# Optimization experiments

Measured on AMD Instinct MI355X. Metric: run time of the kernel, lower is better.

The kernel has to match this reference:

```python
import jax, jax.numpy as jnp
import numpy as np

BETA = 0.25

def setup_inputs() -> dict:
    key = jax.random.key(0)
    k1, k2 = jax.random.split(key)
    z = jax.random.normal(k1, (32, 256, 32, 32), dtype=jnp.float32)
    # embedding init ~ U(-1/K, 1/K) as intended by the module
    K, D = 1024, 256
    codebook = jax.random.uniform(k2, (K, D), dtype=jnp.float32, minval=-1.0 / K, maxval=1.0 / K)
    return {"z": z, "codebook": codebook}


def reference(z, codebook):
    # z: [B, D, H, W] -> [B, H, W, D]
    zt = jnp.transpose(z, (0, 2, 3, 1))
    B, H, W, D = zt.shape
    z_flat = zt.reshape(-1, D)  # [N, D]
    # pairwise squared distance: ||z||^2 + ||e||^2 - 2 z e^T
    dist = (
        jnp.sum(z_flat * z_flat, axis=1, keepdims=True)
        + jnp.sum(codebook * codebook, axis=1)[None, :]
        - 2.0 * jnp.matmul(z_flat, codebook.T)
    )  # [N, K]
    idx = jnp.argmin(dist, axis=1)  # [N]
    z_q = codebook[idx].reshape(B, H, W, D)
    sg = jax.lax.stop_gradient
    loss = jnp.mean((sg(z_q) - zt) ** 2) + BETA * jnp.mean((sg(zt) - z_q) ** 2)
    # straight-through estimator
    z_q = zt + sg(z_q - zt)
    z_q = jnp.transpose(z_q, (0, 3, 1, 2))  # back to [B, D, H, W]
    return z_q, idx, loss
```

## Files before the change

### kernel.cpp

```cpp
#include <hip/hip_runtime.h>


#define D_DIM   256
#define K_CODES 1024
#define HW      1024
#define MT      128
#define NT      256
#define BK      16
#define THREADS 512

#define ZQ_OFF   0
#define IDX_OFF  8388608
#define LOSS_OFF 8421376

#define SMEM_FLOATS (D_DIM*MT + BK*NT + MT + MT)
#define SMEM_BYTES  (SMEM_FLOATS * 4)

extern __shared__ float smem[];

__global__ void enorm_kernel(const float* __restrict__ cb, float* __restrict__ enorm) {
    int gt = blockIdx.x * blockDim.x + threadIdx.x;
    int k = gt >> 6;
    int lane = gt & 63;
    const float4* row = (const float4*)(cb + (size_t)k * D_DIM);
    float4 v = row[lane];
    float s = fmaf(v.x, v.x, fmaf(v.y, v.y, fmaf(v.z, v.z, v.w * v.w)));
    #pragma unroll
    for (int off = 32; off; off >>= 1) s += __shfl_xor(s, off);
    if (lane == 0) enorm[k] = s;
}

__global__ __launch_bounds__(THREADS, 2) void vq_kernel(
        const float* __restrict__ z, const float* __restrict__ cb,
        const float* __restrict__ enorm, float* __restrict__ out)
{
    float* As = smem;
    float* Es = smem + D_DIM * MT;
    int*   bestm   = (int*)(smem + D_DIM*MT + BK*NT);
    float* znorm_s = (float*)(smem + D_DIM*MT + BK*NT + MT);

    const int t   = threadIdx.x;
    const int blk = blockIdx.x;
    const int b   = blk >> 3;
    const int p0  = (blk & 7) * MT;
    const float* zb = z + (size_t)b * D_DIM * HW;

    for (int i = t; i < D_DIM * MT / 4; i += THREADS) {
        int d = i >> 5, m4 = i & 31;
        *(float4*)(As + d * MT + m4 * 4) = *(const float4*)(zb + d * HW + p0 + m4 * 4);
    }
    __syncthreads();

    {
        int m = t & (MT - 1), q = t >> 7;
        const float* col = As + m;
        double zp = 0.0;
        #pragma unroll 8
        for (int d = q * 64; d < q * 64 + 64; ++d) {
            double v = (double)col[d * MT];
            zp += v * v;
        }
        double* zscr = (double*)Es;
        zscr[q * MT + m] = zp;
    }
    __syncthreads();
    if (t < MT) {
        double* zscr = (double*)Es;
        double s = (zscr[t] + zscr[MT + t]) + (zscr[2 * MT + t] + zscr[3 * MT + t]);
        znorm_s[t] = (float)s;
    }
    __syncthreads();

    const int tx = t & 31, ty = t >> 5;
    const int m_base = ty * 8;
    const int kx = tx * 8;

    float znf[8];
    #pragma unroll
    for (int i = 0; i < 8; ++i) znf[i] = znorm_s[m_base + i];

    float bestv[8]; int besti[8];
    #pragma unroll
    for (int i = 0; i < 8; ++i) { bestv[i] = 3.4e38f; besti[i] = 0; }

    for (int c = 0; c < 4; ++c) {
        const int k0 = c * NT;
        float acc[8][8];
        #pragma unroll
        for (int i = 0; i < 8; ++i)
            #pragma unroll
            for (int j = 0; j < 8; ++j) acc[i][j] = 0.f;

        for (int dk = 0; dk < D_DIM; dk += BK) {
            __syncthreads();
            for (int i = t; i < BK * NT / 4; i += THREADS) {
                int kk = i >> 2, d4 = i & 3;
                float4 v = *(const float4*)(cb + (size_t)(k0 + kk) * D_DIM + dk + d4 * 4);
                Es[(d4 * 4 + 0) * NT + kk] = v.x;
                Es[(d4 * 4 + 1) * NT + kk] = v.y;
                Es[(d4 * 4 + 2) * NT + kk] = v.z;
                Es[(d4 * 4 + 3) * NT + kk] = v.w;
            }
            __syncthreads();
            #pragma unroll
            for (int dd = 0; dd < BK; ++dd) {
                float a[8], e[8];
                *(float4*)(a)     = *(const float4*)(As + (dk + dd) * MT + m_base);
                *(float4*)(a + 4) = *(const float4*)(As + (dk + dd) * MT + m_base + 4);
                *(float4*)(e)     = *(const float4*)(Es + dd * NT + kx);
                *(float4*)(e + 4) = *(const float4*)(Es + dd * NT + kx + 4);
                #pragma unroll
                for (int i = 0; i < 8; ++i)
                    #pragma unroll
                    for (int j = 0; j < 8; ++j)
                        acc[i][j] = fmaf(a[i], e[j], acc[i][j]);
            }
        }
        #pragma unroll
        for (int j = 0; j < 8; ++j) {
            float bn = enorm[k0 + kx + j];
            int kidx = k0 + kx + j;
            #pragma unroll
            for (int i = 0; i < 8; ++i) {
                float A   = znf[i] + bn;
                float val = A - 2.0f * acc[i][j];
                if (val < bestv[i] || (val == bestv[i] && kidx < besti[i])) {
                    bestv[i] = val; besti[i] = kidx;
                }
            }
        }
    }

    #pragma unroll
    for (int i = 0; i < 8; ++i) {
        float v = bestv[i]; int ix = besti[i];
        #pragma unroll
        for (int off = 16; off; off >>= 1) {
            float ov = __shfl_xor(v, off);
            int   oi = __shfl_xor(ix, off);
            if (ov < v || (ov == v && oi < ix)) { v = ov; ix = oi; }
        }
        if (tx == 0) {
            bestm[m_base + i] = ix;
            out[IDX_OFF + (size_t)blk * MT + m_base + i] = (float)ix;
        }
    }
    __syncthreads();

    float lsum = 0.f;
    const size_t zq_base = (size_t)b * D_DIM * HW + p0;
    for (int i2 = t; i2 < D_DIM * MT / 4; i2 += THREADS) {
        int p = i2 & (MT - 1), d4 = i2 >> 7;
        int idx = bestm[p];
        float4 cv = *(const float4*)(cb + (size_t)idx * D_DIM + d4 * 4);
        float z0 = As[(d4 * 4 + 0) * MT + p];
        float z1 = As[(d4 * 4 + 1) * MT + p];
        float z2 = As[(d4 * 4 + 2) * MT + p];
        float z3 = As[(d4 * 4 + 3) * MT + p];
        float e0 = cv.x - z0, e1 = cv.y - z1, e2 = cv.z - z2, e3 = cv.w - z3;
        lsum = fmaf(e0, e0, lsum); lsum = fmaf(e1, e1, lsum);
        lsum = fmaf(e2, e2, lsum); lsum = fmaf(e3, e3, lsum);
        out[zq_base + (size_t)(d4 * 4 + 0) * HW + p] = cv.x;
        out[zq_base + (size_t)(d4 * 4 + 1) * HW + p] = cv.y;
        out[zq_base + (size_t)(d4 * 4 + 2) * HW + p] = cv.z;
        out[zq_base + (size_t)(d4 * 4 + 3) * HW + p] = cv.w;
    }
    #pragma unroll
    for (int off = 32; off; off >>= 1) lsum += __shfl_xor(lsum, off);
    __syncthreads();
    if ((t & 63) == 0) Es[t >> 6] = lsum;
    __syncthreads();
    if (t == 0) {
        float s = 0.f;
        #pragma unroll
        for (int w = 0; w < 8; ++w) s += Es[w];
        atomicAdd(out + LOSS_OFF, s * (1.25f / 8388608.f));
    }
}

extern "C" void kernel_launch(void* const* d_in, const int* in_sizes, int n_in,
                              void* d_out, int out_size, void* d_ws, size_t ws_size,
                              hipStream_t stream) {
    const float* z  = (const float*)d_in[0];
    const float* cb = (const float*)d_in[1];
    float* out = (float*)d_out;
    float* enorm = (float*)d_ws;

    hipMemsetAsync(out + LOSS_OFF, 0, sizeof(float), stream);

    enorm_kernel<<<256, 256, 0, stream>>>(cb, enorm);

    hipFuncSetAttribute((const void*)vq_kernel,
                        hipFuncAttributeMaxDynamicSharedMemorySize, SMEM_BYTES);
    vq_kernel<<<256, THREADS, SMEM_BYTES, stream>>>(z, cb, enorm, out);
}
```

Before: 304.3 us.

## Fuse codebook-norm kernel, double threads, and register-prefetch codebook tiles

Removes the separate enorm kernel launch: each block now computes all codebook norms into LDS itself. Doubles the block to 1024 threads, giving each thread an 8x4 accumulator tile instead of 8x8. The codebook tile loop is flattened into 64 steps, with the next tile prefetched into registers while the current one is computed. The LDS tile rows are padded to cut bank conflicts. The cost is redundant norm computation in every block, and the smaller per-thread tile lowers FMA-to-load reuse.

```diff
diff --git a/kernel.cpp b/kernel.cpp
--- a/kernel.cpp
+++ b/kernel.cpp
@@ -6,38 +6,30 @@
 #define HW      1024
 #define MT      128
 #define NT      256
+#define NTP     260
 #define BK      16
-#define THREADS 512
-
-#define ZQ_OFF   0
+#define THREADS 1024
+
 #define IDX_OFF  8388608
 #define LOSS_OFF 8421376
 
-#define SMEM_FLOATS (D_DIM*MT + BK*NT + MT + MT)
+#define AS_F   (D_DIM*MT)
+#define EN_F   (K_CODES)
+#define ES_F   (BK*NTP)
+#define SMEM_FLOATS (AS_F + EN_F + ES_F + MT + MT)
 #define SMEM_BYTES  (SMEM_FLOATS * 4)
 
 extern __shared__ float smem[];
 
-__global__ void enorm_kernel(const float* __restrict__ cb, float* __restrict__ enorm) {
-    int gt = blockIdx.x * blockDim.x + threadIdx.x;
-    int k = gt >> 6;
-    int lane = gt & 63;
-    const float4* row = (const float4*)(cb + (size_t)k * D_DIM);
-    float4 v = row[lane];
-    float s = fmaf(v.x, v.x, fmaf(v.y, v.y, fmaf(v.z, v.z, v.w * v.w)));
-    #pragma unroll
-    for (int off = 32; off; off >>= 1) s += __shfl_xor(s, off);
-    if (lane == 0) enorm[k] = s;
-}
-
-__global__ __launch_bounds__(THREADS, 2) void vq_kernel(
+__global__ __launch_bounds__(THREADS, 4) void vq_kernel(
         const float* __restrict__ z, const float* __restrict__ cb,
-        const float* __restrict__ enorm, float* __restrict__ out)
+        float* __restrict__ out)
 {
-    float* As = smem;
-    float* Es = smem + D_DIM * MT;
-    int*   bestm   = (int*)(smem + D_DIM*MT + BK*NT);
-    float* znorm_s = (float*)(smem + D_DIM*MT + BK*NT + MT);
+    float* As        = smem;
+    float* enorm_lds = smem + AS_F;
+    float* Es        = smem + AS_F + EN_F;
+    int*   bestm     = (int*)(smem + AS_F + EN_F + ES_F);
+    float* znorm_s   = smem + AS_F + EN_F + ES_F + MT;
 
     const int t   = threadIdx.x;
     const int blk = blockIdx.x;
@@ -45,6 +37,10 @@
     const int p0  = (blk & 7) * MT;
     const float* zb = z + (size_t)b * D_DIM * HW;
 
+    const int ek  = t >> 2;
+    const int ed4 = t & 3;
+    float4 vnext = *(const float4*)(cb + (size_t)ek * D_DIM + ed4 * 4);
+
     for (int i = t; i < D_DIM * MT / 4; i += THREADS) {
         int d = i >> 5, m4 = i & 31;
         *(float4*)(As + d * MT + m4 * 4) = *(const float4*)(zb + d * HW + p0 + m4 * 4);
@@ -56,9 +52,9 @@
         const float* col = As + m;
         double zp = 0.0;
         #pragma unroll 8
-        for (int d = q * 64; d < q * 64 + 64; ++d) {
+        for (int d = q * 32; d < q * 32 + 32; ++d) {
             double v = (double)col[d * MT];
-            zp += v * v;
+            zp = fma(v, v, zp);
         }
         double* zscr = (double*)Es;
         zscr[q * MT + m] = zp;
@@ -66,14 +62,28 @@
     __syncthreads();
     if (t < MT) {
         double* zscr = (double*)Es;
-        double s = (zscr[t] + zscr[MT + t]) + (zscr[2 * MT + t] + zscr[3 * MT + t]);
+        double s = ((zscr[t] + zscr[MT + t]) + (zscr[2*MT + t] + zscr[3*MT + t]))
+                 + ((zscr[4*MT + t] + zscr[5*MT + t]) + (zscr[6*MT + t] + zscr[7*MT + t]));
         znorm_s[t] = (float)s;
     }
-    __syncthreads();
-
-    const int tx = t & 31, ty = t >> 5;
+
+    {
+        int w = t >> 6, lane = t & 63;
+        #pragma unroll 4
+        for (int r = 0; r < 64; ++r) {
+            int k = w * 64 + r;
+            float4 v = *(const float4*)(cb + (size_t)k * D_DIM + lane * 4);
+            float s = fmaf(v.x, v.x, fmaf(v.y, v.y, fmaf(v.z, v.z, v.w * v.w)));
+            #pragma unroll
+            for (int off = 32; off; off >>= 1) s += __shfl_xor(s, off);
+            if (lane == 0) enorm_lds[k] = s;
+        }
+    }
+    __syncthreads();
+
+    const int tx = t & 63, ty = t >> 6;
     const int m_base = ty * 8;
-    const int kx = tx * 8;
+    const int kx = tx * 4;
 
     float znf[8];
     #pragma unroll
@@ -83,49 +93,54 @@
     #pragma unroll
     for (int i = 0; i < 8; ++i) { bestv[i] = 3.4e38f; besti[i] = 0; }
 
-    for (int c = 0; c < 4; ++c) {
-        const int k0 = c * NT;
-        float acc[8][8];
+    float acc[8][4];
+
+    for (int s = 0; s < 64; ++s) {
+        __syncthreads();
+        {
+            int r0 = ed4 * 4;
+            Es[(r0 + 0) * NTP + ek] = vnext.x;
+            Es[(r0 + 1) * NTP + ek] = vnext.y;
+            Es[(r0 + 2) * NTP + ek] = vnext.z;
+            Es[(r0 + 3) * NTP + ek] = vnext.w;
+        }
+        __syncthreads();
+        if (s < 63) {
+            int s1 = s + 1, c1 = s1 >> 4, dk1 = (s1 & 15) * BK;
+            vnext = *(const float4*)(cb + (size_t)(c1 * NT + ek) * D_DIM + dk1 + ed4 * 4);
+        }
+        if ((s & 15) == 0) {
+            #pragma unroll
+            for (int i = 0; i < 8; ++i)
+                #pragma unroll
+                for (int j = 0; j < 4; ++j) acc[i][j] = 0.f;
+        }
+        const int dka = (s & 15) * BK;
         #pragma unroll
-        for (int i = 0; i < 8; ++i)
-            #pragma unroll
-            for (int j = 0; j < 8; ++j) acc[i][j] = 0.f;
-
-        for (int dk = 0; dk < D_DIM; dk += BK) {
-            __syncthreads();
-            for (int i = t; i < BK * NT / 4; i += THREADS) {
-                int kk = i >> 2, d4 = i & 3;
-                float4 v = *(const float4*)(cb + (size_t)(k0 + kk) * D_DIM + dk + d4 * 4);
-                Es[(d4 * 4 + 0) * NT + kk] = v.x;
-                Es[(d4 * 4 + 1) * NT + kk] = v.y;
-                Es[(d4 * 4 + 2) * NT + kk] = v.z;
-                Es[(d4 * 4 + 3) * NT + kk] = v.w;
-            }
-            __syncthreads();
-            #pragma unroll
-            for (int dd = 0; dd < BK; ++dd) {
-                float a[8], e[8];
-                *(float4*)(a)     = *(const float4*)(As + (dk + dd) * MT + m_base);
-                *(float4*)(a + 4) = *(const float4*)(As + (dk + dd) * MT + m_base + 4);
-                *(float4*)(e)     = *(const float4*)(Es + dd * NT + kx);
-                *(float4*)(e + 4) = *(const float4*)(Es + dd * NT + kx + 4);
+        for (int dd = 0; dd < BK; ++dd) {
+            float a[8], e[4];
+            *(float4*)(a)     = *(const float4*)(As + (dka + dd) * MT + m_base);
+            *(float4*)(a + 4) = *(const float4*)(As + (dka + dd) * MT + m_base + 4);
+            *(float4*)(e)     = *(const float4*)(Es + dd * NTP + kx);
+            #pragma unroll
+            for (int i = 0; i < 8; ++i)
                 #pragma unroll
-                for (int i = 0; i < 8; ++i)
-                    #pragma unroll
-                    for (int j = 0; j < 8; ++j)
-                        acc[i][j] = fmaf(a[i], e[j], acc[i][j]);
-            }
-        }
-        #pragma unroll
-        for (int j = 0; j < 8; ++j) {
-            float bn = enorm[k0 + kx + j];
-            int kidx = k0 + kx + j;
-            #pragma unroll
-            for (int i = 0; i < 8; ++i) {
-                float A   = znf[i] + bn;
-                float val = A - 2.0f * acc[i][j];
-                if (val < bestv[i] || (val == bestv[i] && kidx < besti[i])) {
-                    bestv[i] = val; besti[i] = kidx;
+                for (int j = 0; j < 4; ++j)
+                    acc[i][j] = fmaf(a[i], e[j], acc[i][j]);
+        }
+        if ((s & 15) == 15) {
+            int k0 = (s >> 4) * NT;
+            #pragma unroll
+            for (int j = 0; j < 4; ++j) {
+                float bn = enorm_lds[k0 + kx + j];
+                int kidx = k0 + kx + j;
+                #pragma unroll
+                for (int i = 0; i < 8; ++i) {
+                    float A   = znf[i] + bn;
+                    float val = A - 2.0f * acc[i][j];
+                    if (val < bestv[i] || (val == bestv[i] && kidx < besti[i])) {
+                        bestv[i] = val; besti[i] = kidx;
+                    }
                 }
             }
         }
@@ -135,7 +150,7 @@
     for (int i = 0; i < 8; ++i) {
         float v = bestv[i]; int ix = besti[i];
         #pragma unroll
-        for (int off = 16; off; off >>= 1) {
+        for (int off = 32; off; off >>= 1) {
             float ov = __shfl_xor(v, off);
             int   oi = __shfl_xor(ix, off);
             if (ov < v || (ov == v && oi < ix)) { v = ov; ix = oi; }
@@ -171,10 +186,10 @@
     if ((t & 63) == 0) Es[t >> 6] = lsum;
     __syncthreads();
     if (t == 0) {
-        float s = 0.f;
+        float ssum = 0.f;
         #pragma unroll
-        for (int w = 0; w < 8; ++w) s += Es[w];
-        atomicAdd(out + LOSS_OFF, s * (1.25f / 8388608.f));
+        for (int w = 0; w < 16; ++w) ssum += Es[w];
+        atomicAdd(out + LOSS_OFF, ssum * (1.25f / 8388608.f));
     }
 }
 
@@ -184,13 +199,10 @@
     const float* z  = (const float*)d_in[0];
     const float* cb = (const float*)d_in[1];
     float* out = (float*)d_out;
-    float* enorm = (float*)d_ws;
 
     hipMemsetAsync(out + LOSS_OFF, 0, sizeof(float), stream);
-
-    enorm_kernel<<<256, 256, 0, stream>>>(cb, enorm);
 
     hipFuncSetAttribute((const void*)vq_kernel,
                         hipFuncAttributeMaxDynamicSharedMemorySize, SMEM_BYTES);
-    vq_kernel<<<256, THREADS, SMEM_BYTES, stream>>>(z, cb, enorm, out);
+    vq_kernel<<<256, THREADS, SMEM_BYTES, stream>>>(z, cb, out);
 }
```

Result: slower. 448.2 us (+47.3%).
